# Kernel tuning notes

Hardware: AMD Instinct MI355X
Metric: run time of the kernel (lower is better)

Reference implementation:

```python
import jax, jax.numpy as jnp
import numpy as np
from jax import lax

N_T, B, C_IN, H, W = 24, 2, 9, 32, 32   # n timesteps, batch, bands, tile HxW
N_FILTER, KM, N_CLASS, HID = 32, 16, 10, 128


def setup_inputs() -> dict:
    key = jax.random.key(0)
    ks = jax.random.split(key, 6)
    x = jax.random.normal(ks[0], (N_T, B, C_IN, H, W), jnp.float32)
    kernels = jax.random.normal(ks[1], (N_FILTER, KM, C_IN), jnp.float32)  # DTW filter kernels
    W1 = jax.random.normal(ks[2], (N_FILTER, HID), jnp.float32) * 0.1
    b1 = jnp.zeros((HID,), jnp.float32)
    W2 = jax.random.normal(ks[3], (HID, HID), jnp.float32) * 0.1
    b2 = jnp.zeros((HID,), jnp.float32)
    Wl = jax.random.normal(ks[4], (HID, N_CLASS), jnp.float32) * 0.1
    bl = jnp.zeros((N_CLASS,), jnp.float32)
    return {"x": x, "kernels": kernels, "W1": W1, "b1": b1, "W2": W2, "b2": b2, "Wl": Wl, "bl": bl}


def _dtw_single(kernel, seq):
    # kernel: (m, c), seq: (n, c). Classic DTW with squared-euclidean local cost,
    # then sum of local costs along the optimal alignment path (path is non-diff,
    # matching the torch code's detached dtw_path + differentiable squared diffs).
    C = jnp.sum((kernel[:, None, :] - seq[None, :, :]) ** 2, axis=-1)  # (m, n)
    m, n = C.shape
    inf = jnp.array(jnp.inf, C.dtype)
    row0 = jnp.cumsum(C[0])

    def row_step(prev, crow):
        prev_shift = jnp.concatenate([jnp.full((1,), inf, C.dtype), prev[:-1]])
        def col_step(left, cud):
            c, up, diag = cud
            d = c + jnp.minimum(left, jnp.minimum(up, diag))
            return d, d
        _, row = lax.scan(col_step, inf, (crow, prev, prev_shift))
        return row, row

    _, rows = lax.scan(row_step, row0, C[1:])
    D = lax.stop_gradient(jnp.concatenate([row0[None, :], rows], axis=0))  # (m, n)

    def bt_step(carry, _):
        i, j, acc, done = carry
        im1 = jnp.maximum(i - 1, 0)
        jm1 = jnp.maximum(j - 1, 0)
        cand = jnp.stack([
            jnp.where((i > 0) & (j > 0), D[im1, jm1], inf),  # diagonal
            jnp.where(i > 0, D[im1, j], inf),                # up
            jnp.where(j > 0, D[i, jm1], inf)])               # left
        choice = jnp.argmin(cand)  # first-min tie-break = diagonal preferred (as np.argmin)
        ni = jnp.where(choice == 2, i, im1)
        nj = jnp.where(choice == 1, j, jm1)
        ni = jnp.where(done, i, ni)
        nj = jnp.where(done, j, nj)
        acc = acc + jnp.where(done, jnp.array(0.0, C.dtype), C[ni, nj])
        done = done | ((ni == 0) & (nj == 0))
        return (ni, nj, acc, done), None

    init = (jnp.int32(m - 1), jnp.int32(n - 1), C[m - 1, n - 1], jnp.array(m == 1 and n == 1))
    (_, _, total, _), _ = lax.scan(bt_step, init, None, length=m + n - 2)
    return total


def reference(x, kernels, W1, b1, W2, b2, Wl, bl):
    n, b, c, h, w = x.shape
    # torch.cat(list_of_n, dim=0).view(-1, n, c) == row-major reshape of (n,b,c,h,w)
    seqs = x.reshape(-1, n, c)  # (B2, n, c), B2 = b*h*w
    feats = jax.vmap(lambda s: jax.vmap(lambda k: _dtw_single(k, s))(kernels))(seqs)  # (B2, F)
    t = jax.nn.relu(feats @ W1 + b1)
    t = jax.nn.relu(t @ W2 + b2)
    t = jax.nn.softmax(t @ Wl + bl, axis=1)
    return t.reshape(b, N_CLASS, h, w)
```

## Files before the change

kernel.cpp:

```cpp
#include <hip/hip_runtime.h>

#define NT   24
#define CIN  9
#define NF   32
#define KM   16
#define HID  128
#define NCLS 10
#define SEQ_LEN (NT*CIN)
#define PADJ 12
#define NSTRIP 4

__global__ __launch_bounds__(128, 4) void dtwnet_fused(
    const float* __restrict__ x,
    const float* __restrict__ kern,
    const float* __restrict__ W1, const float* __restrict__ b1,
    const float* __restrict__ W2, const float* __restrict__ b2,
    const float* __restrict__ Wl, const float* __restrict__ bl,
    float* __restrict__ out)
{
  __shared__ float seq_lds[NT*PADJ];
  __shared__ float bcol[NT];
  __shared__ float feat_lds[NF];
  __shared__ float h1_lds[HID];
  __shared__ float h2_lds[HID];
  __shared__ float logit_lds[NCLS];

  const int tid  = threadIdx.x;
  const int bid  = blockIdx.x;
  const int wave = tid >> 6;
  const int lane = tid & 63;
  const int s    = lane >> 4;
  const int f_lo = lane & 15;
  const int f    = wave*16 + f_lo;

  float kf[4*CIN];
  {
    const float4* kp = (const float4*)(kern + f*(KM*CIN) + s*(4*CIN));
    float4 t0 = kp[0], t1 = kp[1], t2 = kp[2], t3 = kp[3], t4 = kp[4],
           t5 = kp[5], t6 = kp[6], t7 = kp[7], t8 = kp[8];
    kf[0]=t0.x; kf[1]=t0.y; kf[2]=t0.z; kf[3]=t0.w;
    kf[4]=t1.x; kf[5]=t1.y; kf[6]=t1.z; kf[7]=t1.w;
    kf[8]=t2.x; kf[9]=t2.y; kf[10]=t2.z; kf[11]=t2.w;
    kf[12]=t3.x; kf[13]=t3.y; kf[14]=t3.z; kf[15]=t3.w;
    kf[16]=t4.x; kf[17]=t4.y; kf[18]=t4.z; kf[19]=t4.w;
    kf[20]=t5.x; kf[21]=t5.y; kf[22]=t5.z; kf[23]=t5.w;
    kf[24]=t6.x; kf[25]=t6.y; kf[26]=t6.z; kf[27]=t6.w;
    kf[28]=t7.x; kf[29]=t7.y; kf[30]=t7.z; kf[31]=t7.w;
    kf[32]=t8.x; kf[33]=t8.y; kf[34]=t8.z; kf[35]=t8.w;
  }

  for (int d = tid; d < SEQ_LEN; d += 128) {
    int jj = d / CIN, cc = d - jj*CIN;
    seq_lds[jj*PADJ + cc] = x[bid*SEQ_LEN + d];
  }
  __syncthreads();

  if (tid < NT) {
    const float4* sp = (const float4*)(seq_lds + tid*PADJ);
    float4 q0 = sp[0], q1 = sp[1], q2 = sp[2];
    float b = q0.x*q0.x + q0.y*q0.y + q0.z*q0.z + q0.w*q0.w
            + q1.x*q1.x + q1.y*q1.y + q1.z*q1.z + q1.w*q1.w
            + q2.x*q2.x;
    bcol[tid] = b;
  }

  float arow[4];
  #pragma unroll
  for (int r = 0; r < 4; ++r) {
    float a = 0.f;
    #pragma unroll
    for (int c = 0; c < CIN; ++c) a = fmaf(kf[r*CIN+c], kf[r*CIN+c], a);
    arow[r] = a;
  }
  #pragma unroll
  for (int q = 0; q < 4*CIN; ++q) kf[q] *= -2.f;
  __syncthreads();

  float rowD[4];
  float bndUp = 0.f, bndDg = 0.f;

  #pragma unroll 1
  for (int t = 0; t < NT + NSTRIP - 1; ++t) {
    int j = t - s;
    bool active = (j >= 0) && (j < NT);
    float nb = 0.f;
    if (active) {
      const float4* sp = (const float4*)(seq_lds + j*PADJ);
      float4 q0 = sp[0], q1 = sp[1], q2 = sp[2];
      float bj = bcol[j];
      float sv[CIN] = {q0.x,q0.y,q0.z,q0.w,q1.x,q1.y,q1.z,q1.w,q2.x};
      float cost[4];
      #pragma unroll
      for (int r = 0; r < 4; ++r) {
        float cc = arow[r] + bj;
        #pragma unroll
        for (int c = 0; c < CIN; ++c) cc = fmaf(kf[r*CIN+c], sv[c], cc);
        cost[r] = cc;
      }
      if (j == 0) {
        float acc = (s == 0) ? 0.f : bndUp;
        #pragma unroll
        for (int r = 0; r < 4; ++r) { acc += cost[r]; rowD[r] = acc; }
      } else {
        float up, diag;
        float left = rowD[0];
        float D0;
        if (s == 0) {
          D0 = cost[0] + left;
        } else {
          D0 = cost[0] + fminf(bndDg, fminf(bndUp, left));
        }
        diag = left;
        rowD[0] = D0; up = D0;
        #pragma unroll
        for (int r = 1; r < 4; ++r) {
          float lD = rowD[r];
          float D2 = cost[r] + fminf(diag, fminf(up, lD));
          diag = lD;
          rowD[r] = D2; up = D2;
        }
      }
      nb = rowD[3];
    }
    float rD = __shfl_up(nb, 16u);
    bndDg = bndUp;
    bndUp = rD;
  }

  if (s == 3) feat_lds[f] = rowD[3];
  __syncthreads();

  {
    float acc = b1[tid];
    #pragma unroll
    for (int k = 0; k < NF; ++k) acc = fmaf(feat_lds[k], W1[k*HID + tid], acc);
    h1_lds[tid] = fmaxf(acc, 0.f);
  }
  __syncthreads();
  {
    const float4* hh = (const float4*)h1_lds;
    float a0 = b2[tid], a1 = 0.f, a2 = 0.f, a3 = 0.f;
    #pragma unroll
    for (int k = 0; k < HID/4; ++k) {
      float4 h4 = hh[k];
      a0 = fmaf(h4.x, W2[(4*k+0)*HID + tid], a0);
      a1 = fmaf(h4.y, W2[(4*k+1)*HID + tid], a1);
      a2 = fmaf(h4.z, W2[(4*k+2)*HID + tid], a2);
      a3 = fmaf(h4.w, W2[(4*k+3)*HID + tid], a3);
    }
    h2_lds[tid] = fmaxf((a0 + a1) + (a2 + a3), 0.f);
  }
  __syncthreads();
  if (tid < NCLS) {
    const float4* hh = (const float4*)h2_lds;
    float a0 = bl[tid], a1 = 0.f, a2 = 0.f, a3 = 0.f;
    #pragma unroll
    for (int k = 0; k < HID/4; ++k) {
      float4 h4 = hh[k];
      a0 = fmaf(h4.x, Wl[(4*k+0)*NCLS + tid], a0);
      a1 = fmaf(h4.y, Wl[(4*k+1)*NCLS + tid], a1);
      a2 = fmaf(h4.z, Wl[(4*k+2)*NCLS + tid], a2);
      a3 = fmaf(h4.w, Wl[(4*k+3)*NCLS + tid], a3);
    }
    logit_lds[tid] = (a0 + a1) + (a2 + a3);
  }
  __syncthreads();
  if (tid == 0) {
    float mx = logit_lds[0];
    #pragma unroll
    for (int j = 1; j < NCLS; ++j) mx = fmaxf(mx, logit_lds[j]);
    float e[NCLS]; float sum = 0.f;
    #pragma unroll
    for (int j = 0; j < NCLS; ++j) { e[j] = __expf(logit_lds[j] - mx); sum += e[j]; }
    float inv = 1.f / sum;
    float* op = out + bid*NCLS;
    #pragma unroll
    for (int j = 0; j < NCLS; ++j) op[j] = e[j] * inv;
  }
}

extern "C" void kernel_launch(void* const* d_in, const int* in_sizes, int n_in,
                              void* d_out, int out_size, void* d_ws, size_t ws_size,
                              hipStream_t stream) {
  const float* x    = (const float*)d_in[0];
  const float* kern = (const float*)d_in[1];
  const float* W1   = (const float*)d_in[2];
  const float* b1   = (const float*)d_in[3];
  const float* W2   = (const float*)d_in[4];
  const float* b2   = (const float*)d_in[5];
  const float* Wl   = (const float*)d_in[6];
  const float* bl   = (const float*)d_in[7];
  float* out = (float*)d_out;

  dtwnet_fused<<<2048, 128, 0, stream>>>(x, kern, W1, b1, W2, b2, Wl, bl, out);
}
```

Before: 83.61 us.

## Process four sequences per block with one thread computing a full DTW column

Each block now handles four pixel sequences, and each thread owns one filter and runs the whole 16-row DTW recurrence itself. This removes the wavefront strip decomposition and its shuffles. The MLP head is batched over the four sequences so each W1/W2 load is reused four times. The grid shrinks to 512 blocks, and each thread holds 144 kernel values plus 16 DP values in registers, so register pressure rises and occupancy falls.

```diff
diff --git a/kernel.cpp b/kernel.cpp
--- a/kernel.cpp
+++ b/kernel.cpp
@@ -8,9 +8,9 @@
 #define NCLS 10
 #define SEQ_LEN (NT*CIN)
 #define PADJ 12
-#define NSTRIP 4
-
-__global__ __launch_bounds__(128, 4) void dtwnet_fused(
+#define GSEQ 4
+
+__global__ __launch_bounds__(128, 1) void dtwnet_fused(
     const float* __restrict__ x,
     const float* __restrict__ kern,
     const float* __restrict__ W1, const float* __restrict__ b1,
@@ -18,164 +18,192 @@
     const float* __restrict__ Wl, const float* __restrict__ bl,
     float* __restrict__ out)
 {
-  __shared__ float seq_lds[NT*PADJ];
-  __shared__ float bcol[NT];
-  __shared__ float feat_lds[NF];
-  __shared__ float h1_lds[HID];
-  __shared__ float h2_lds[HID];
-  __shared__ float logit_lds[NCLS];
-
-  const int tid  = threadIdx.x;
-  const int bid  = blockIdx.x;
-  const int wave = tid >> 6;
-  const int lane = tid & 63;
-  const int s    = lane >> 4;
-  const int f_lo = lane & 15;
-  const int f    = wave*16 + f_lo;
-
-  float kf[4*CIN];
-  {
-    const float4* kp = (const float4*)(kern + f*(KM*CIN) + s*(4*CIN));
-    float4 t0 = kp[0], t1 = kp[1], t2 = kp[2], t3 = kp[3], t4 = kp[4],
-           t5 = kp[5], t6 = kp[6], t7 = kp[7], t8 = kp[8];
-    kf[0]=t0.x; kf[1]=t0.y; kf[2]=t0.z; kf[3]=t0.w;
-    kf[4]=t1.x; kf[5]=t1.y; kf[6]=t1.z; kf[7]=t1.w;
-    kf[8]=t2.x; kf[9]=t2.y; kf[10]=t2.z; kf[11]=t2.w;
-    kf[12]=t3.x; kf[13]=t3.y; kf[14]=t3.z; kf[15]=t3.w;
-    kf[16]=t4.x; kf[17]=t4.y; kf[18]=t4.z; kf[19]=t4.w;
-    kf[20]=t5.x; kf[21]=t5.y; kf[22]=t5.z; kf[23]=t5.w;
-    kf[24]=t6.x; kf[25]=t6.y; kf[26]=t6.z; kf[27]=t6.w;
-    kf[28]=t7.x; kf[29]=t7.y; kf[30]=t7.z; kf[31]=t7.w;
-    kf[32]=t8.x; kf[33]=t8.y; kf[34]=t8.z; kf[35]=t8.w;
-  }
-
-  for (int d = tid; d < SEQ_LEN; d += 128) {
-    int jj = d / CIN, cc = d - jj*CIN;
-    seq_lds[jj*PADJ + cc] = x[bid*SEQ_LEN + d];
-  }
-  __syncthreads();
-
-  if (tid < NT) {
-    const float4* sp = (const float4*)(seq_lds + tid*PADJ);
+  __shared__ float seq_lds[GSEQ][NT*PADJ];
+  __shared__ float bcol[GSEQ][NT];
+  __shared__ float feat[GSEQ][NF];
+  __shared__ float h1[GSEQ][HID];
+  __shared__ float h2[GSEQ][HID];
+  __shared__ float logit_lds[GSEQ][NCLS];
+
+  const int tid = threadIdx.x;
+  const int bid = blockIdx.x;
+  const int g   = tid >> 5;
+  const int f   = tid & 31;
+
+  float kf[KM*CIN];
+  {
+    const float4* kp = (const float4*)(kern + f*(KM*CIN));
+    #pragma unroll
+    for (int i = 0; i < (KM*CIN)/4; ++i) {
+      float4 t = kp[i];
+      kf[4*i+0]=t.x; kf[4*i+1]=t.y; kf[4*i+2]=t.z; kf[4*i+3]=t.w;
+    }
+  }
+
+  #pragma unroll
+  for (int it = 0; it < 7; ++it) {
+    int d = tid + it*128;
+    if (d < GSEQ*SEQ_LEN) {
+      int gg  = d / SEQ_LEN;
+      int rem = d - gg*SEQ_LEN;
+      int jj  = rem / CIN;
+      int cc  = rem - jj*CIN;
+      seq_lds[gg][jj*PADJ + cc] = x[(bid*GSEQ + gg)*SEQ_LEN + rem];
+    }
+  }
+
+  float arow[KM];
+  #pragma unroll
+  for (int r = 0; r < KM; ++r) {
+    float a = 0.f;
+    #pragma unroll
+    for (int c = 0; c < CIN; ++c) a = fmaf(kf[r*CIN+c], kf[r*CIN+c], a);
+    arow[r] = a;
+  }
+  #pragma unroll
+  for (int q = 0; q < KM*CIN; ++q) kf[q] *= -2.f;
+
+  __syncthreads();
+
+  if (tid < GSEQ*NT) {
+    int gg = tid / NT;
+    int jj = tid - gg*NT;
+    const float4* sp = (const float4*)(&seq_lds[gg][jj*PADJ]);
     float4 q0 = sp[0], q1 = sp[1], q2 = sp[2];
     float b = q0.x*q0.x + q0.y*q0.y + q0.z*q0.z + q0.w*q0.w
             + q1.x*q1.x + q1.y*q1.y + q1.z*q1.z + q1.w*q1.w
             + q2.x*q2.x;
-    bcol[tid] = b;
-  }
-
-  float arow[4];
-  #pragma unroll
-  for (int r = 0; r < 4; ++r) {
-    float a = 0.f;
-    #pragma unroll
-    for (int c = 0; c < CIN; ++c) a = fmaf(kf[r*CIN+c], kf[r*CIN+c], a);
-    arow[r] = a;
-  }
-  #pragma unroll
-  for (int q = 0; q < 4*CIN; ++q) kf[q] *= -2.f;
-  __syncthreads();
-
-  float rowD[4];
-  float bndUp = 0.f, bndDg = 0.f;
-
-  #pragma unroll 1
-  for (int t = 0; t < NT + NSTRIP - 1; ++t) {
-    int j = t - s;
-    bool active = (j >= 0) && (j < NT);
-    float nb = 0.f;
-    if (active) {
-      const float4* sp = (const float4*)(seq_lds + j*PADJ);
-      float4 q0 = sp[0], q1 = sp[1], q2 = sp[2];
-      float bj = bcol[j];
-      float sv[CIN] = {q0.x,q0.y,q0.z,q0.w,q1.x,q1.y,q1.z,q1.w,q2.x};
-      float cost[4];
+    bcol[gg][jj] = b;
+  }
+  __syncthreads();
+
+  const float* scol = &seq_lds[g][0];
+  float rowD[KM];
+  {
+    const float4* sp = (const float4*)scol;
+    float4 q0 = sp[0], q1 = sp[1], q2 = sp[2];
+    float sv[CIN] = {q0.x,q0.y,q0.z,q0.w,q1.x,q1.y,q1.z,q1.w,q2.x};
+    float bj = bcol[g][0];
+    float acc = 0.f;
+    #pragma unroll
+    for (int r = 0; r < KM; ++r) {
+      float cc = arow[r] + bj;
       #pragma unroll
-      for (int r = 0; r < 4; ++r) {
-        float cc = arow[r] + bj;
-        #pragma unroll
-        for (int c = 0; c < CIN; ++c) cc = fmaf(kf[r*CIN+c], sv[c], cc);
-        cost[r] = cc;
-      }
-      if (j == 0) {
-        float acc = (s == 0) ? 0.f : bndUp;
-        #pragma unroll
-        for (int r = 0; r < 4; ++r) { acc += cost[r]; rowD[r] = acc; }
-      } else {
-        float up, diag;
-        float left = rowD[0];
-        float D0;
-        if (s == 0) {
-          D0 = cost[0] + left;
-        } else {
-          D0 = cost[0] + fminf(bndDg, fminf(bndUp, left));
-        }
-        diag = left;
-        rowD[0] = D0; up = D0;
-        #pragma unroll
-        for (int r = 1; r < 4; ++r) {
-          float lD = rowD[r];
-          float D2 = cost[r] + fminf(diag, fminf(up, lD));
-          diag = lD;
-          rowD[r] = D2; up = D2;
-        }
-      }
-      nb = rowD[3];
-    }
-    float rD = __shfl_up(nb, 16u);
-    bndDg = bndUp;
-    bndUp = rD;
-  }
-
-  if (s == 3) feat_lds[f] = rowD[3];
-  __syncthreads();
-
-  {
-    float acc = b1[tid];
-    #pragma unroll
-    for (int k = 0; k < NF; ++k) acc = fmaf(feat_lds[k], W1[k*HID + tid], acc);
-    h1_lds[tid] = fmaxf(acc, 0.f);
-  }
-  __syncthreads();
-  {
-    const float4* hh = (const float4*)h1_lds;
-    float a0 = b2[tid], a1 = 0.f, a2 = 0.f, a3 = 0.f;
-    #pragma unroll
-    for (int k = 0; k < HID/4; ++k) {
-      float4 h4 = hh[k];
-      a0 = fmaf(h4.x, W2[(4*k+0)*HID + tid], a0);
-      a1 = fmaf(h4.y, W2[(4*k+1)*HID + tid], a1);
-      a2 = fmaf(h4.z, W2[(4*k+2)*HID + tid], a2);
-      a3 = fmaf(h4.w, W2[(4*k+3)*HID + tid], a3);
-    }
-    h2_lds[tid] = fmaxf((a0 + a1) + (a2 + a3), 0.f);
-  }
-  __syncthreads();
-  if (tid < NCLS) {
-    const float4* hh = (const float4*)h2_lds;
-    float a0 = bl[tid], a1 = 0.f, a2 = 0.f, a3 = 0.f;
-    #pragma unroll
-    for (int k = 0; k < HID/4; ++k) {
-      float4 h4 = hh[k];
-      a0 = fmaf(h4.x, Wl[(4*k+0)*NCLS + tid], a0);
-      a1 = fmaf(h4.y, Wl[(4*k+1)*NCLS + tid], a1);
-      a2 = fmaf(h4.z, Wl[(4*k+2)*NCLS + tid], a2);
-      a3 = fmaf(h4.w, Wl[(4*k+3)*NCLS + tid], a3);
-    }
-    logit_lds[tid] = (a0 + a1) + (a2 + a3);
-  }
-  __syncthreads();
-  if (tid == 0) {
-    float mx = logit_lds[0];
-    #pragma unroll
-    for (int j = 1; j < NCLS; ++j) mx = fmaxf(mx, logit_lds[j]);
+      for (int c = 0; c < CIN; ++c) cc = fmaf(kf[r*CIN+c], sv[c], cc);
+      acc += cc;
+      rowD[r] = acc;
+    }
+  }
+  #pragma unroll 2
+  for (int j = 1; j < NT; ++j) {
+    const float4* sp = (const float4*)(scol + j*PADJ);
+    float4 q0 = sp[0], q1 = sp[1], q2 = sp[2];
+    float sv[CIN] = {q0.x,q0.y,q0.z,q0.w,q1.x,q1.y,q1.z,q1.w,q2.x};
+    float bj = bcol[g][j];
+    float nD[KM];
+    {
+      float cc = arow[0] + bj;
+      #pragma unroll
+      for (int c = 0; c < CIN; ++c) cc = fmaf(kf[c], sv[c], cc);
+      nD[0] = cc + rowD[0];
+    }
+    #pragma unroll
+    for (int r = 1; r < KM; ++r) {
+      float cc = arow[r] + bj;
+      #pragma unroll
+      for (int c = 0; c < CIN; ++c) cc = fmaf(kf[r*CIN+c], sv[c], cc);
+      nD[r] = cc + fminf(rowD[r], fminf(nD[r-1], rowD[r-1]));
+    }
+    #pragma unroll
+    for (int r = 0; r < KM; ++r) rowD[r] = nD[r];
+  }
+
+  feat[g][f] = rowD[KM-1];
+  __syncthreads();
+
+  {
+    float b1v = b1[tid];
+    float a0 = b1v, a1 = b1v, a2 = b1v, a3 = b1v;
+    const float4* f0 = (const float4*)&feat[0][0];
+    const float4* f1 = (const float4*)&feat[1][0];
+    const float4* f2 = (const float4*)&feat[2][0];
+    const float4* f3 = (const float4*)&feat[3][0];
+    #pragma unroll
+    for (int k4 = 0; k4 < NF/4; ++k4) {
+      float4 v0 = f0[k4], v1 = f1[k4], v2 = f2[k4], v3 = f3[k4];
+      float w0 = W1[(4*k4+0)*HID + tid];
+      float w1 = W1[(4*k4+1)*HID + tid];
+      float w2 = W1[(4*k4+2)*HID + tid];
+      float w3 = W1[(4*k4+3)*HID + tid];
+      a0 = fmaf(v0.x,w0,a0); a0 = fmaf(v0.y,w1,a0); a0 = fmaf(v0.z,w2,a0); a0 = fmaf(v0.w,w3,a0);
+      a1 = fmaf(v1.x,w0,a1); a1 = fmaf(v1.y,w1,a1); a1 = fmaf(v1.z,w2,a1); a1 = fmaf(v1.w,w3,a1);
+      a2 = fmaf(v2.x,w0,a2); a2 = fmaf(v2.y,w1,a2); a2 = fmaf(v2.z,w2,a2); a2 = fmaf(v2.w,w3,a2);
+      a3 = fmaf(v3.x,w0,a3); a3 = fmaf(v3.y,w1,a3); a3 = fmaf(v3.z,w2,a3); a3 = fmaf(v3.w,w3,a3);
+    }
+    h1[0][tid] = fmaxf(a0, 0.f);
+    h1[1][tid] = fmaxf(a1, 0.f);
+    h1[2][tid] = fmaxf(a2, 0.f);
+    h1[3][tid] = fmaxf(a3, 0.f);
+  }
+  __syncthreads();
+
+  {
+    float b2v = b2[tid];
+    float p00=b2v, p01=0.f, p02=0.f, p03=0.f;
+    float p10=b2v, p11=0.f, p12=0.f, p13=0.f;
+    float p20=b2v, p21=0.f, p22=0.f, p23=0.f;
+    float p30=b2v, p31=0.f, p32=0.f, p33=0.f;
+    const float4* q0p = (const float4*)&h1[0][0];
+    const float4* q1p = (const float4*)&h1[1][0];
+    const float4* q2p = (const float4*)&h1[2][0];
+    const float4* q3p = (const float4*)&h1[3][0];
+    #pragma unroll
+    for (int k4 = 0; k4 < HID/4; ++k4) {
+      float4 v0 = q0p[k4], v1 = q1p[k4], v2 = q2p[k4], v3 = q3p[k4];
+      float w0 = W2[(4*k4+0)*HID + tid];
+      float w1 = W2[(4*k4+1)*HID + tid];
+      float w2 = W2[(4*k4+2)*HID + tid];
+      float w3 = W2[(4*k4+3)*HID + tid];
+      p00 = fmaf(v0.x,w0,p00); p01 = fmaf(v0.y,w1,p01); p02 = fmaf(v0.z,w2,p02); p03 = fmaf(v0.w,w3,p03);
+      p10 = fmaf(v1.x,w0,p10); p11 = fmaf(v1.y,w1,p11); p12 = fmaf(v1.z,w2,p12); p13 = fmaf(v1.w,w3,p13);
+      p20 = fmaf(v2.x,w0,p20); p21 = fmaf(v2.y,w1,p21); p22 = fmaf(v2.z,w2,p22); p23 = fmaf(v2.w,w3,p23);
+      p30 = fmaf(v3.x,w0,p30); p31 = fmaf(v3.y,w1,p31); p32 = fmaf(v3.z,w2,p32); p33 = fmaf(v3.w,w3,p33);
+    }
+    h2[0][tid] = fmaxf((p00+p01)+(p02+p03), 0.f);
+    h2[1][tid] = fmaxf((p10+p11)+(p12+p13), 0.f);
+    h2[2][tid] = fmaxf((p20+p21)+(p22+p23), 0.f);
+    h2[3][tid] = fmaxf((p30+p31)+(p32+p33), 0.f);
+  }
+  __syncthreads();
+
+  if (tid < GSEQ*NCLS) {
+    int gg = tid / NCLS;
+    int c  = tid - gg*NCLS;
+    const float4* hh = (const float4*)&h2[gg][0];
+    float a0 = bl[c], a1 = 0.f, a2 = 0.f, a3 = 0.f;
+    #pragma unroll
+    for (int k4 = 0; k4 < HID/4; ++k4) {
+      float4 h4 = hh[k4];
+      a0 = fmaf(h4.x, Wl[(4*k4+0)*NCLS + c], a0);
+      a1 = fmaf(h4.y, Wl[(4*k4+1)*NCLS + c], a1);
+      a2 = fmaf(h4.z, Wl[(4*k4+2)*NCLS + c], a2);
+      a3 = fmaf(h4.w, Wl[(4*k4+3)*NCLS + c], a3);
+    }
+    logit_lds[gg][c] = (a0 + a1) + (a2 + a3);
+  }
+  __syncthreads();
+
+  if (tid < GSEQ) {
+    float mx = logit_lds[tid][0];
+    #pragma unroll
+    for (int jj = 1; jj < NCLS; ++jj) mx = fmaxf(mx, logit_lds[tid][jj]);
     float e[NCLS]; float sum = 0.f;
     #pragma unroll
-    for (int j = 0; j < NCLS; ++j) { e[j] = __expf(logit_lds[j] - mx); sum += e[j]; }
+    for (int jj = 0; jj < NCLS; ++jj) { e[jj] = __expf(logit_lds[tid][jj] - mx); sum += e[jj]; }
     float inv = 1.f / sum;
-    float* op = out + bid*NCLS;
-    #pragma unroll
-    for (int j = 0; j < NCLS; ++j) op[j] = e[j] * inv;
+    float* op = out + (bid*GSEQ + tid)*NCLS;
+    #pragma unroll
+    for (int jj = 0; jj < NCLS; ++jj) op[jj] = e[jj] * inv;
   }
 }
 
@@ -192,5 +220,5 @@
   const float* bl   = (const float*)d_in[7];
   float* out = (float*)d_out;
 
-  dtwnet_fused<<<2048, 128, 0, stream>>>(x, kern, W1, b1, W2, b2, Wl, bl, out);
+  dtwnet_fused<<<512, 128, 0, stream>>>(x, kern, W1, b1, W2, b2, Wl, bl, out);
 }
```

New measurement: 87.85 us. 5.1% more time.
